# Kernel optimization log

Measured on AMD Instinct MI355X. Metric: run time of the kernel, lower is better.

## Reference

```python
import jax, jax.numpy as jnp
import numpy as np

N_FEAT = 512
N_HEAD = 8
D_K = N_FEAT // N_HEAD


def setup_inputs() -> dict:
    key = jax.random.key(0)
    ks = jax.random.split(key, 10)
    B, S = 2, 4096
    scale = 1.0 / np.sqrt(N_FEAT)
    inp = {
        "x": jax.random.normal(ks[0], (B, S, N_FEAT), dtype=jnp.float32),
        "mask": jnp.zeros((B, 1, 1, S), dtype=jnp.float32),
        "wq": jax.random.normal(ks[1], (N_FEAT, N_FEAT), dtype=jnp.float32) * scale,
        "bq": jnp.zeros((N_FEAT,), dtype=jnp.float32),
        "wk": jax.random.normal(ks[2], (N_FEAT, N_FEAT), dtype=jnp.float32) * scale,
        "bk": jnp.zeros((N_FEAT,), dtype=jnp.float32),
        "wv": jax.random.normal(ks[3], (N_FEAT, N_FEAT), dtype=jnp.float32) * scale,
        "bv": jnp.zeros((N_FEAT,), dtype=jnp.float32),
        "wo": jax.random.normal(ks[4], (N_FEAT, N_FEAT), dtype=jnp.float32) * scale,
        "bo": jnp.zeros((N_FEAT,), dtype=jnp.float32),
    }
    return inp


def reference(x, mask, wq, bq, wk, bk, wv, bv, wo, bo):
    B, S, _ = x.shape
    # QKV projections (weights stored [in, out] = W^T of torch Linear)
    def proj(w, b):
        y = x @ w + b                      # [B, S, n_feat]
        y = y.reshape(B, S, N_HEAD, D_K)
        return y.transpose(0, 2, 1, 3)     # [B, H, S, d_k]
    q = proj(wq, bq)
    k = proj(wk, bk)
    v = proj(wv, bv)
    scores = jnp.einsum("bhsd,bhtd->bhst", q, k) / jnp.sqrt(jnp.float32(D_K))
    scores = scores + mask                 # additive mask, broadcast [B,1,1,S]
    attn = jax.nn.softmax(scores, axis=-1) # [B, H, S, S]
    ctx = jnp.einsum("bhst,bhtd->bhsd", attn, v)
    ctx = ctx.transpose(0, 2, 1, 3).reshape(B, S, N_FEAT)
    return ctx @ wo + bo
```

## Files before the change

kernel.cpp:

```cpp
#include <hip/hip_runtime.h>
#include <hip/hip_bf16.h>
#include <math.h>

#define SLEN 4096
#define NF   512
#define LOG2E 1.44269504f

typedef short s8v  __attribute__((ext_vector_type(8)));
typedef short s4v  __attribute__((ext_vector_type(4)));
typedef float f4v  __attribute__((ext_vector_type(4)));
typedef float f16v __attribute__((ext_vector_type(16)));
typedef __attribute__((address_space(1))) const unsigned int gu32;
typedef __attribute__((address_space(3))) unsigned int lu32;

static __device__ __forceinline__ short f2bf(float f) {
  union { float f; unsigned int u; } v; v.f = f;
  unsigned int u = v.u;
  unsigned int r = (u + 0x7FFFu + ((u >> 16) & 1u)) >> 16;
  return (short)r;
}

__global__ __launch_bounds__(256) void prep_all(
    const float* __restrict__ x, const float* __restrict__ bq,
    const float* __restrict__ mask,
    short* __restrict__ xb, float* __restrict__ bqs, float* __restrict__ maskl) {
  const int b = blockIdx.x, tid = threadIdx.x;
  if (b < 2048) {
    size_t i = ((size_t)b * 256 + tid) * 8;
    float4 a = *(const float4*)(x + i);
    float4 c = *(const float4*)(x + i + 4);
    s8v o;
    o[0] = f2bf(a.x); o[1] = f2bf(a.y); o[2] = f2bf(a.z); o[3] = f2bf(a.w);
    o[4] = f2bf(c.x); o[5] = f2bf(c.y); o[6] = f2bf(c.z); o[7] = f2bf(c.w);
    *(s8v*)(xb + i) = o;
  } else if (b == 2048) {
#pragma unroll
    for (int j = 0; j < 2; j++) {
      int i = tid + 256 * j;
      bqs[i] = bq[i] * (0.125f * LOG2E);
    }
  } else {
    int i4 = ((b - 2049) * 1024) + tid * 4;
    float4 m = *(const float4*)(mask + i4);
    m.x *= LOG2E; m.y *= LOG2E; m.z *= LOG2E; m.w *= LOG2E;
    *(float4*)(maskl + i4) = m;
  }
}

__global__ __launch_bounds__(256) void prep_w(
    const float* __restrict__ wq, const float* __restrict__ wk,
    const float* __restrict__ wv, const float* __restrict__ wo,
    short* __restrict__ wt) {
  const int bz = blockIdx.y;
  const float* W = (bz == 0) ? wq : (bz == 1) ? wk : (bz == 2) ? wv : wo;
  const float scale = (bz == 0) ? 0.125f * LOG2E : 1.0f;
  const int tk = blockIdx.x & 7, tn = blockIdx.x >> 3;
  __shared__ short T[64][68];
  const int tid = threadIdx.x;
#pragma unroll
  for (int p = 0; p < 4; p++) {
    int c = tid + 256 * p;
    int kk = c >> 4, c4 = c & 15;
    float4 v = *(const float4*)(W + (size_t)(tk * 64 + kk) * NF + tn * 64 + c4 * 4);
    T[kk][c4 * 4 + 0] = f2bf(v.x * scale);
    T[kk][c4 * 4 + 1] = f2bf(v.y * scale);
    T[kk][c4 * 4 + 2] = f2bf(v.z * scale);
    T[kk][c4 * 4 + 3] = f2bf(v.w * scale);
  }
  __syncthreads();
#pragma unroll
  for (int p = 0; p < 2; p++) {
    int c = tid + 256 * p;
    int nrow = c >> 3, ks = c & 7;
    s8v g;
#pragma unroll
    for (int j = 0; j < 8; j++) g[j] = T[ks * 8 + j][nrow];
    *(s8v*)(wt + (size_t)bz * NF * NF + (size_t)(tn * 64 + nrow) * NF + tk * 64 + ks * 8) = g;
  }
}

__global__ __launch_bounds__(256) void qkv_proj(
    const short* __restrict__ xb, const short* __restrict__ wt,
    const float* __restrict__ bqs, const float* __restrict__ bk,
    const float* __restrict__ bv,
    short* __restrict__ qo, short* __restrict__ ko, short* __restrict__ vo)
{
  const int z = blockIdx.z;
  const short* WT   = wt + (size_t)z * NF * NF;
  const float* bias = (z == 0) ? bqs : (z == 1) ? bk : bv;
  const int m0 = blockIdx.x * 128;
  const int n0 = blockIdx.y * 128;

  __shared__ short Al[2][128][32];
  __shared__ short Bl[2][128][32];

  const int tid = threadIdx.x;
  const int wave = tid >> 6, lane = tid & 63;
  const int lg = lane >> 4, lr = lane & 15;
  const int wm = wave >> 1, wn = wave & 1;

  const int grow = lane >> 2;
  const int gsl  = lane & 3;

  f4v acc[4][4];
#pragma unroll
  for (int i = 0; i < 4; i++)
#pragma unroll
    for (int j = 0; j < 4; j++) acc[i][j] = (f4v){0.f, 0.f, 0.f, 0.f};

#pragma unroll
  for (int c = 0; c < 2; c++) {
    int row = wave * 32 + c * 16 + grow;
    __builtin_amdgcn_global_load_lds(
        (gu32*)(xb + (size_t)(m0 + row) * NF + gsl * 8),
        (lu32*)&Al[0][wave * 32 + c * 16][0], 16, 0, 0);
    __builtin_amdgcn_global_load_lds(
        (gu32*)(WT + (size_t)(n0 + row) * NF + gsl * 8),
        (lu32*)&Bl[0][wave * 32 + c * 16][0], 16, 0, 0);
  }

#pragma unroll
  for (int ki = 0; ki < 16; ki++) {
    const int cur = ki & 1;
    __syncthreads();

    if (ki + 1 < 16) {
      const int kn = (ki + 1) * 32;
#pragma unroll
      for (int c = 0; c < 2; c++) {
        int row = wave * 32 + c * 16 + grow;
        __builtin_amdgcn_global_load_lds(
            (gu32*)(xb + (size_t)(m0 + row) * NF + kn + gsl * 8),
            (lu32*)&Al[cur ^ 1][wave * 32 + c * 16][0], 16, 0, 0);
        __builtin_amdgcn_global_load_lds(
            (gu32*)(WT + (size_t)(n0 + row) * NF + kn + gsl * 8),
            (lu32*)&Bl[cur ^ 1][wave * 32 + c * 16][0], 16, 0, 0);
      }
    }

    s8v af[4], bf[4];
#pragma unroll
    for (int f = 0; f < 4; f++) af[f] = *(const s8v*)&Al[cur][wm * 64 + f * 16 + lr][lg * 8];
#pragma unroll
    for (int f = 0; f < 4; f++) bf[f] = *(const s8v*)&Bl[cur][wn * 64 + f * 16 + lr][lg * 8];
#pragma unroll
    for (int i = 0; i < 4; i++)
#pragma unroll
      for (int j = 0; j < 4; j++)
        acc[i][j] = __builtin_amdgcn_mfma_f32_16x16x32_bf16(af[i], bf[j], acc[i][j], 0, 0, 0);
  }

#pragma unroll
  for (int i = 0; i < 4; i++) {
    int mbase = m0 + wm * 64 + i * 16 + lg * 4;
#pragma unroll
    for (int j = 0; j < 4; j++) {
      int n = n0 + wn * 64 + j * 16 + lr;
      float bval = bias[n];
      int h = n >> 6, d = n & 63;
      if (z == 2) {
        int b = mbase >> 12, s = mbase & 4095;
        s4v pk;
#pragma unroll
        for (int r = 0; r < 4; r++) pk[r] = f2bf(acc[i][j][r] + bval);
        *(s4v*)(vo + ((size_t)((b * 8 + h) * 64 + d)) * SLEN + s) = pk;
      } else {
        short* dst = (z == 0) ? qo : ko;
#pragma unroll
        for (int r = 0; r < 4; r++) {
          int m = mbase + r;
          int b = m >> 12, s = m & 4095;
          dst[((size_t)((b * 8 + h)) * SLEN + s) * 64 + d] = f2bf(acc[i][j][r] + bval);
        }
      }
    }
  }
}

template<int SPLIT>
__global__ __launch_bounds__(256) void attn(
    const short* __restrict__ q, const short* __restrict__ k,
    const short* __restrict__ vt, const float* __restrict__ maskl,
    short* __restrict__ ctx, float* __restrict__ poa, float* __restrict__ plc)
{
  const int KVLEN = SLEN / SPLIT;
  const int NT = KVLEN / 64;
  __shared__ short Kl[2][64][64];
  __shared__ short Vl[2][64][64];

  const int tid = threadIdx.x;
  const int wave = tid >> 6, lane = tid & 63;
  const int h = lane >> 5, ln = lane & 31;

  const int x = blockIdx.x;
  const int c8 = x & 7, idx = x >> 3;
  const int bhsp = c8 + 8 * (idx >> 5);
  const int qb = idx & 31;
  const int bh = bhsp & 15;
  const int sp = bhsp >> 4;
  const int bb = bh >> 3, hh = bh & 7;
  const int q0 = qb * 128 + wave * 32;

  const short* qp = q + ((size_t)bh * SLEN + q0 + ln) * 64 + h * 8;
  s8v qf[4];
#pragma unroll
  for (int d = 0; d < 4; d++) qf[d] = *(const s8v*)(qp + d * 16);

  s8v ones;
#pragma unroll
  for (int j = 0; j < 8; j++) ones[j] = (short)0x3F80;

  f16v oa[2], lacc;
#pragma unroll
  for (int i = 0; i < 16; i++) { oa[0][i] = 0.f; oa[1][i] = 0.f; lacc[i] = 0.f; }

  const short* kg = k + (size_t)bh * SLEN * 64 + (size_t)sp * KVLEN * 64;
  const short* vg = vt + (size_t)bh * 64 * SLEN + (size_t)sp * KVLEN;
  const float* mp = maskl + (size_t)bb * SLEN + (size_t)sp * KVLEN;

  const int srow = tid >> 3, ss = tid & 7;
  const int sws = (ss ^ (srow & 7)) * 8;

  s8v kr0 = *(const s8v*)(kg + (size_t)srow * 64 + ss * 8);
  s8v kr1 = *(const s8v*)(kg + (size_t)(srow + 32) * 64 + ss * 8);
  s8v vr0 = *(const s8v*)(vg + (size_t)srow * SLEN + ss * 8);
  s8v vr1 = *(const s8v*)(vg + (size_t)(srow + 32) * SLEN + ss * 8);
  *(s8v*)&Kl[0][srow][sws] = kr0;  *(s8v*)&Kl[0][srow + 32][sws] = kr1;
  *(s8v*)&Vl[0][srow][sws] = vr0;  *(s8v*)&Vl[0][srow + 32][sws] = vr1;

  for (int it = 0; it < NT; ++it) {
    const int cur = it & 1;
    const int t0 = it * 64;
    __syncthreads();

    if (it + 1 < NT) {
      kr0 = *(const s8v*)(kg + (size_t)(t0 + 64 + srow) * 64 + ss * 8);
      kr1 = *(const s8v*)(kg + (size_t)(t0 + 96 + srow) * 64 + ss * 8);
      vr0 = *(const s8v*)(vg + (size_t)srow * SLEN + t0 + 64 + ss * 8);
      vr1 = *(const s8v*)(vg + (size_t)(srow + 32) * SLEN + t0 + 64 + ss * 8);
    }

    f16v sa[2];
#pragma unroll
    for (int tt = 0; tt < 2; tt++) {
#pragma unroll
      for (int q4 = 0; q4 < 4; q4++) {
        float4 mv = *(const float4*)(mp + t0 + tt * 32 + q4 * 8 + h * 4);
        sa[tt][q4 * 4 + 0] = mv.x;
        sa[tt][q4 * 4 + 1] = mv.y;
        sa[tt][q4 * 4 + 2] = mv.z;
        sa[tt][q4 * 4 + 3] = mv.w;
      }
    }
    __builtin_amdgcn_s_setprio(1);
#pragma unroll
    for (int tt = 0; tt < 2; tt++) {
#pragma unroll
      for (int ds_ = 0; ds_ < 4; ds_++) {
        s8v kf = *(const s8v*)&Kl[cur][tt * 32 + ln][(((ds_ * 2 + h) ^ (ln & 7))) * 8];
        sa[tt] = __builtin_amdgcn_mfma_f32_32x32x16_bf16(kf, qf[ds_], sa[tt], 0, 0, 0);
      }
    }
    __builtin_amdgcn_s_setprio(0);

    unsigned int pku[2][4][2];
#pragma unroll
    for (int tt = 0; tt < 2; tt++)
#pragma unroll
      for (int q4 = 0; q4 < 4; q4++) {
        float p0, p1, p2, p3;
        asm("v_exp_f32 %0, %1" : "=v"(p0) : "v"(sa[tt][q4 * 4 + 0]));
        asm("v_exp_f32 %0, %1" : "=v"(p1) : "v"(sa[tt][q4 * 4 + 1]));
        asm("v_exp_f32 %0, %1" : "=v"(p2) : "v"(sa[tt][q4 * 4 + 2]));
        asm("v_exp_f32 %0, %1" : "=v"(p3) : "v"(sa[tt][q4 * 4 + 3]));
        unsigned int u0, u1;
        asm("v_cvt_pk_bf16_f32 %0, %1, %2" : "=v"(u0) : "v"(p0), "v"(p1));
        asm("v_cvt_pk_bf16_f32 %0, %1, %2" : "=v"(u1) : "v"(p2), "v"(p3));
        pku[tt][q4][0] = u0;
        pku[tt][q4][1] = u1;
      }

    __builtin_amdgcn_s_setprio(1);
#pragma unroll
    for (int ks = 0; ks < 4; ks++) {
      const int tt = ks >> 1, k1 = ks & 1;
      unsigned int s0 = h ? pku[tt][2 * k1][0] : pku[tt][2 * k1 + 1][0];
      unsigned int s1 = h ? pku[tt][2 * k1][1] : pku[tt][2 * k1 + 1][1];
      unsigned int r0 = (unsigned int)__shfl_xor((int)s0, 32);
      unsigned int r1 = (unsigned int)__shfl_xor((int)s1, 32);
      union { unsigned int u[4]; s8v v; } af;
      af.u[0] = h ? r0 : pku[tt][2 * k1][0];
      af.u[1] = h ? r1 : pku[tt][2 * k1][1];
      af.u[2] = h ? pku[tt][2 * k1 + 1][0] : r0;
      af.u[3] = h ? pku[tt][2 * k1 + 1][1] : r1;
      lacc = __builtin_amdgcn_mfma_f32_32x32x16_bf16(af.v, ones, lacc, 0, 0, 0);
#pragma unroll
      for (int dt = 0; dt < 2; dt++) {
        s8v vf = *(const s8v*)&Vl[cur][dt * 32 + ln][(((ks * 2 + h) ^ (ln & 7))) * 8];
        oa[dt] = __builtin_amdgcn_mfma_f32_32x32x16_bf16(af.v, vf, oa[dt], 0, 0, 0);
      }
    }
    __builtin_amdgcn_s_setprio(0);

    if (it + 1 < NT) {
      *(s8v*)&Kl[cur ^ 1][srow][sws] = kr0;  *(s8v*)&Kl[cur ^ 1][srow + 32][sws] = kr1;
      *(s8v*)&Vl[cur ^ 1][srow][sws] = vr0;  *(s8v*)&Vl[cur ^ 1][srow + 32][sws] = vr1;
    }
  }

  if constexpr (SPLIT == 1) {
#pragma unroll
    for (int q4 = 0; q4 < 4; q4++)
#pragma unroll
      for (int i = 0; i < 4; i++) {
        float inv = 1.0f / lacc[q4 * 4 + i];
        int qrow = q0 + i + q4 * 8 + 4 * h;
        size_t base = ((size_t)bb * SLEN + qrow) * NF + hh * 64;
        ctx[base + ln]      = f2bf(oa[0][q4 * 4 + i] * inv);
        ctx[base + 32 + ln] = f2bf(oa[1][q4 * 4 + i] * inv);
      }
  } else {
#pragma unroll
    for (int dt = 0; dt < 2; dt++) {
      size_t dbase = ((size_t)(sp * 16 + bh) * 64 + dt * 32 + ln) * SLEN;
#pragma unroll
      for (int q4 = 0; q4 < 4; q4++) {
        float4 v = {oa[dt][q4 * 4 + 0], oa[dt][q4 * 4 + 1],
                    oa[dt][q4 * 4 + 2], oa[dt][q4 * 4 + 3]};
        *(float4*)(poa + dbase + q0 + q4 * 8 + 4 * h) = v;
      }
    }
    if (ln == 0) {
      size_t lbase = (size_t)(sp * 16 + bh) * SLEN;
#pragma unroll
      for (int q4 = 0; q4 < 4; q4++) {
        float4 v = {lacc[q4 * 4 + 0], lacc[q4 * 4 + 1],
                    lacc[q4 * 4 + 2], lacc[q4 * 4 + 3]};
        *(float4*)(plc + lbase + q0 + q4 * 8 + 4 * h) = v;
      }
    }
  }
}

__global__ __launch_bounds__(256) void out_proj(
    const short* __restrict__ ctx, const short* __restrict__ wt,
    const float* __restrict__ bo, float* __restrict__ out)
{
  const short* WT = wt + (size_t)3 * NF * NF;
  const int m0 = blockIdx.x * 128;
  const int n0 = blockIdx.y * 128;
  __shared__ short Al[2][128][32];
  __shared__ short Bl[2][128][32];
  const int tid = threadIdx.x;
  const int wave = tid >> 6, lane = tid & 63;
  const int lg = lane >> 4, lr = lane & 15;
  const int wm = wave >> 1, wn = wave & 1;
  const int grow = lane >> 2;
  const int gsl  = lane & 3;

  f4v acc[4][4];
#pragma unroll
  for (int i = 0; i < 4; i++)
#pragma unroll
    for (int j = 0; j < 4; j++) acc[i][j] = (f4v){0.f, 0.f, 0.f, 0.f};

#pragma unroll
  for (int c = 0; c < 2; c++) {
    int row = wave * 32 + c * 16 + grow;
    __builtin_amdgcn_global_load_lds(
        (gu32*)(ctx + (size_t)(m0 + row) * NF + gsl * 8),
        (lu32*)&Al[0][wave * 32 + c * 16][0], 16, 0, 0);
    __builtin_amdgcn_global_load_lds(
        (gu32*)(WT + (size_t)(n0 + row) * NF + gsl * 8),
        (lu32*)&Bl[0][wave * 32 + c * 16][0], 16, 0, 0);
  }

#pragma unroll
  for (int ki = 0; ki < 16; ki++) {
    const int cur = ki & 1;
    __syncthreads();

    if (ki + 1 < 16) {
      const int kn = (ki + 1) * 32;
#pragma unroll
      for (int c = 0; c < 2; c++) {
        int row = wave * 32 + c * 16 + grow;
        __builtin_amdgcn_global_load_lds(
            (gu32*)(ctx + (size_t)(m0 + row) * NF + kn + gsl * 8),
            (lu32*)&Al[cur ^ 1][wave * 32 + c * 16][0], 16, 0, 0);
        __builtin_amdgcn_global_load_lds(
            (gu32*)(WT + (size_t)(n0 + row) * NF + kn + gsl * 8),
            (lu32*)&Bl[cur ^ 1][wave * 32 + c * 16][0], 16, 0, 0);
      }
    }

    s8v af[4], bf[4];
#pragma unroll
    for (int f = 0; f < 4; f++) af[f] = *(const s8v*)&Al[cur][wm * 64 + f * 16 + lr][lg * 8];
#pragma unroll
    for (int f = 0; f < 4; f++) bf[f] = *(const s8v*)&Bl[cur][wn * 64 + f * 16 + lr][lg * 8];
#pragma unroll
    for (int i = 0; i < 4; i++)
#pragma unroll
      for (int j = 0; j < 4; j++)
        acc[i][j] = __builtin_amdgcn_mfma_f32_16x16x32_bf16(af[i], bf[j], acc[i][j], 0, 0, 0);
  }

#pragma unroll
  for (int i = 0; i < 4; i++) {
    int mbase = m0 + wm * 64 + i * 16 + lg * 4;
#pragma unroll
    for (int j = 0; j < 4; j++) {
      int n = n0 + wn * 64 + j * 16 + lr;
      float bval = bo[n];
#pragma unroll
      for (int r = 0; r < 4; r++)
        out[(size_t)(mbase + r) * NF + n] = acc[i][j][r] + bval;
    }
  }
}

extern "C" void kernel_launch(void* const* d_in, const int* in_sizes, int n_in,
                              void* d_out, int out_size, void* d_ws, size_t ws_size,
                              hipStream_t stream) {
  const float* x    = (const float*)d_in[0];
  const float* mask = (const float*)d_in[1];
  const float* wq   = (const float*)d_in[2];
  const float* bq   = (const float*)d_in[3];
  const float* wk   = (const float*)d_in[4];
  const float* bk   = (const float*)d_in[5];
  const float* wv   = (const float*)d_in[6];
  const float* bv   = (const float*)d_in[7];
  const float* wo   = (const float*)d_in[8];
  const float* bo   = (const float*)d_in[9];
  float* out = (float*)d_out;

  char* ws = (char*)d_ws;
  const size_t MB = 1024ull * 1024ull;
  short* xb    = (short*)(ws);
  short* q_ws  = (short*)(ws + 8 * MB);
  short* k_ws  = (short*)(ws + 16 * MB);
  short* v_ws  = (short*)(ws + 24 * MB);
  short* c_ws  = (short*)(ws + 32 * MB);
  short* wt    = (short*)(ws + 40 * MB);
  float* bqs   = (float*)(ws + 42 * MB);
  float* maskl = (float*)(ws + 43 * MB);
  float* poa   = (float*)(ws + 44 * MB);
  float* plc   = (float*)(ws + 76 * MB);

  prep_all<<<2057, 256, 0, stream>>>(x, bq, mask, xb, bqs, maskl);
  prep_w<<<dim3(64, 4), 256, 0, stream>>>(wq, wk, wv, wo, wt);
  qkv_proj<<<dim3(64, 4, 3), 256, 0, stream>>>(xb, wt, bqs, bk, bv, q_ws, k_ws, v_ws);
  attn<1><<<512, 256, 0, stream>>>(q_ws, k_ws, v_ws, maskl, c_ws, poa, plc);
  out_proj<<<dim3(64, 4), 256, 0, stream>>>(c_ws, wt, bo, out);
}
```

Measured before the change: 148.6 us.

## Use 128-key attention tiles and merge weight prep into prep_all launch

The attention kernel now stages 128 keys per iteration instead of 64, so there are half as many loop iterations and block barriers. Each tile is processed as two 64-key halves, with the next tile's prefetch split across those halves. The weight transpose/convert kernel is folded into prep_all as extra blocks, removing one kernel launch. In exchange, shared memory per block doubles (to 64KB), which may lower occupancy, and the XOR swizzle on the 128-wide V rows only covers 8 of the 16 chunks.

```diff
diff --git a/kernel.cpp b/kernel.cpp
--- a/kernel.cpp
+++ b/kernel.cpp
@@ -23,7 +23,11 @@
 __global__ __launch_bounds__(256) void prep_all(
     const float* __restrict__ x, const float* __restrict__ bq,
     const float* __restrict__ mask,
-    short* __restrict__ xb, float* __restrict__ bqs, float* __restrict__ maskl) {
+    const float* __restrict__ wq, const float* __restrict__ wk,
+    const float* __restrict__ wv, const float* __restrict__ wo,
+    short* __restrict__ xb, float* __restrict__ bqs,
+    float* __restrict__ maskl, short* __restrict__ wt) {
+  __shared__ short T[64][68];
   const int b = blockIdx.x, tid = threadIdx.x;
   if (b < 2048) {
     size_t i = ((size_t)b * 256 + tid) * 8;
@@ -39,43 +43,37 @@
       int i = tid + 256 * j;
       bqs[i] = bq[i] * (0.125f * LOG2E);
     }
-  } else {
+  } else if (b < 2057) {
     int i4 = ((b - 2049) * 1024) + tid * 4;
     float4 m = *(const float4*)(mask + i4);
     m.x *= LOG2E; m.y *= LOG2E; m.z *= LOG2E; m.w *= LOG2E;
     *(float4*)(maskl + i4) = m;
-  }
-}
-
-__global__ __launch_bounds__(256) void prep_w(
-    const float* __restrict__ wq, const float* __restrict__ wk,
-    const float* __restrict__ wv, const float* __restrict__ wo,
-    short* __restrict__ wt) {
-  const int bz = blockIdx.y;
-  const float* W = (bz == 0) ? wq : (bz == 1) ? wk : (bz == 2) ? wv : wo;
-  const float scale = (bz == 0) ? 0.125f * LOG2E : 1.0f;
-  const int tk = blockIdx.x & 7, tn = blockIdx.x >> 3;
-  __shared__ short T[64][68];
-  const int tid = threadIdx.x;
-#pragma unroll
-  for (int p = 0; p < 4; p++) {
-    int c = tid + 256 * p;
-    int kk = c >> 4, c4 = c & 15;
-    float4 v = *(const float4*)(W + (size_t)(tk * 64 + kk) * NF + tn * 64 + c4 * 4);
-    T[kk][c4 * 4 + 0] = f2bf(v.x * scale);
-    T[kk][c4 * 4 + 1] = f2bf(v.y * scale);
-    T[kk][c4 * 4 + 2] = f2bf(v.z * scale);
-    T[kk][c4 * 4 + 3] = f2bf(v.w * scale);
-  }
-  __syncthreads();
-#pragma unroll
-  for (int p = 0; p < 2; p++) {
-    int c = tid + 256 * p;
-    int nrow = c >> 3, ks = c & 7;
-    s8v g;
-#pragma unroll
-    for (int j = 0; j < 8; j++) g[j] = T[ks * 8 + j][nrow];
-    *(s8v*)(wt + (size_t)bz * NF * NF + (size_t)(tn * 64 + nrow) * NF + tk * 64 + ks * 8) = g;
+  } else {
+    const int bp = b - 2057;
+    const int bz = bp >> 6, t = bp & 63;
+    const float* W = (bz == 0) ? wq : (bz == 1) ? wk : (bz == 2) ? wv : wo;
+    const float scale = (bz == 0) ? 0.125f * LOG2E : 1.0f;
+    const int tk = t & 7, tn = t >> 3;
+#pragma unroll
+    for (int p = 0; p < 4; p++) {
+      int c = tid + 256 * p;
+      int kk = c >> 4, c4 = c & 15;
+      float4 v = *(const float4*)(W + (size_t)(tk * 64 + kk) * NF + tn * 64 + c4 * 4);
+      T[kk][c4 * 4 + 0] = f2bf(v.x * scale);
+      T[kk][c4 * 4 + 1] = f2bf(v.y * scale);
+      T[kk][c4 * 4 + 2] = f2bf(v.z * scale);
+      T[kk][c4 * 4 + 3] = f2bf(v.w * scale);
+    }
+    __syncthreads();
+#pragma unroll
+    for (int p = 0; p < 2; p++) {
+      int c = tid + 256 * p;
+      int nrow = c >> 3, ks = c & 7;
+      s8v g;
+#pragma unroll
+      for (int j = 0; j < 8; j++) g[j] = T[ks * 8 + j][nrow];
+      *(s8v*)(wt + (size_t)bz * NF * NF + (size_t)(tn * 64 + nrow) * NF + tk * 64 + ks * 8) = g;
+    }
   }
 }
 
@@ -98,7 +96,6 @@
   const int wave = tid >> 6, lane = tid & 63;
   const int lg = lane >> 4, lr = lane & 15;
   const int wm = wave >> 1, wn = wave & 1;
-
   const int grow = lane >> 2;
   const int gsl  = lane & 3;
 
@@ -184,9 +181,9 @@
     short* __restrict__ ctx, float* __restrict__ poa, float* __restrict__ plc)
 {
   const int KVLEN = SLEN / SPLIT;
-  const int NT = KVLEN / 64;
-  __shared__ short Kl[2][64][64];
-  __shared__ short Vl[2][64][64];
+  const int NT = KVLEN / 128;
+  __shared__ short Kl[2][128][64];
+  __shared__ short Vl[2][64][128];
 
   const int tid = threadIdx.x;
   const int wave = tid >> 6, lane = tid & 63;
@@ -218,93 +215,104 @@
   const short* vg = vt + (size_t)bh * 64 * SLEN + (size_t)sp * KVLEN;
   const float* mp = maskl + (size_t)bb * SLEN + (size_t)sp * KVLEN;
 
-  const int srow = tid >> 3, ss = tid & 7;
-  const int sws = (ss ^ (srow & 7)) * 8;
-
-  s8v kr0 = *(const s8v*)(kg + (size_t)srow * 64 + ss * 8);
-  s8v kr1 = *(const s8v*)(kg + (size_t)(srow + 32) * 64 + ss * 8);
-  s8v vr0 = *(const s8v*)(vg + (size_t)srow * SLEN + ss * 8);
-  s8v vr1 = *(const s8v*)(vg + (size_t)(srow + 32) * SLEN + ss * 8);
-  *(s8v*)&Kl[0][srow][sws] = kr0;  *(s8v*)&Kl[0][srow + 32][sws] = kr1;
-  *(s8v*)&Vl[0][srow][sws] = vr0;  *(s8v*)&Vl[0][srow + 32][sws] = vr1;
+  const int tk = tid >> 3, sk = tid & 7;
+  const int dv = tid >> 4, sv = tid & 15;
+  const int swsk = (sk ^ (tk & 7)) * 8;
+  const int swsv = (sv ^ (dv & 7)) * 8;
+
+#pragma unroll
+  for (int p = 0; p < 4; p++) {
+    s8v kr = *(const s8v*)(kg + (size_t)(p * 32 + tk) * 64 + sk * 8);
+    *(s8v*)&Kl[0][p * 32 + tk][swsk] = kr;
+    s8v vr = *(const s8v*)(vg + (size_t)(p * 16 + dv) * SLEN + sv * 8);
+    *(s8v*)&Vl[0][p * 16 + dv][swsv] = vr;
+  }
 
   for (int it = 0; it < NT; ++it) {
     const int cur = it & 1;
-    const int t0 = it * 64;
+    const int t0 = it * 128;
     __syncthreads();
 
-    if (it + 1 < NT) {
-      kr0 = *(const s8v*)(kg + (size_t)(t0 + 64 + srow) * 64 + ss * 8);
-      kr1 = *(const s8v*)(kg + (size_t)(t0 + 96 + srow) * 64 + ss * 8);
-      vr0 = *(const s8v*)(vg + (size_t)srow * SLEN + t0 + 64 + ss * 8);
-      vr1 = *(const s8v*)(vg + (size_t)(srow + 32) * SLEN + t0 + 64 + ss * 8);
-    }
-
-    f16v sa[2];
-#pragma unroll
-    for (int tt = 0; tt < 2; tt++) {
-#pragma unroll
-      for (int q4 = 0; q4 < 4; q4++) {
-        float4 mv = *(const float4*)(mp + t0 + tt * 32 + q4 * 8 + h * 4);
-        sa[tt][q4 * 4 + 0] = mv.x;
-        sa[tt][q4 * 4 + 1] = mv.y;
-        sa[tt][q4 * 4 + 2] = mv.z;
-        sa[tt][q4 * 4 + 3] = mv.w;
-      }
-    }
-    __builtin_amdgcn_s_setprio(1);
-#pragma unroll
-    for (int tt = 0; tt < 2; tt++) {
-#pragma unroll
-      for (int ds_ = 0; ds_ < 4; ds_++) {
-        s8v kf = *(const s8v*)&Kl[cur][tt * 32 + ln][(((ds_ * 2 + h) ^ (ln & 7))) * 8];
-        sa[tt] = __builtin_amdgcn_mfma_f32_32x32x16_bf16(kf, qf[ds_], sa[tt], 0, 0, 0);
-      }
-    }
-    __builtin_amdgcn_s_setprio(0);
-
-    unsigned int pku[2][4][2];
-#pragma unroll
-    for (int tt = 0; tt < 2; tt++)
-#pragma unroll
-      for (int q4 = 0; q4 < 4; q4++) {
-        float p0, p1, p2, p3;
-        asm("v_exp_f32 %0, %1" : "=v"(p0) : "v"(sa[tt][q4 * 4 + 0]));
-        asm("v_exp_f32 %0, %1" : "=v"(p1) : "v"(sa[tt][q4 * 4 + 1]));
-        asm("v_exp_f32 %0, %1" : "=v"(p2) : "v"(sa[tt][q4 * 4 + 2]));
-        asm("v_exp_f32 %0, %1" : "=v"(p3) : "v"(sa[tt][q4 * 4 + 3]));
-        unsigned int u0, u1;
-        asm("v_cvt_pk_bf16_f32 %0, %1, %2" : "=v"(u0) : "v"(p0), "v"(p1));
-        asm("v_cvt_pk_bf16_f32 %0, %1, %2" : "=v"(u1) : "v"(p2), "v"(p3));
-        pku[tt][q4][0] = u0;
-        pku[tt][q4][1] = u1;
-      }
-
-    __builtin_amdgcn_s_setprio(1);
-#pragma unroll
-    for (int ks = 0; ks < 4; ks++) {
-      const int tt = ks >> 1, k1 = ks & 1;
-      unsigned int s0 = h ? pku[tt][2 * k1][0] : pku[tt][2 * k1 + 1][0];
-      unsigned int s1 = h ? pku[tt][2 * k1][1] : pku[tt][2 * k1 + 1][1];
-      unsigned int r0 = (unsigned int)__shfl_xor((int)s0, 32);
-      unsigned int r1 = (unsigned int)__shfl_xor((int)s1, 32);
-      union { unsigned int u[4]; s8v v; } af;
-      af.u[0] = h ? r0 : pku[tt][2 * k1][0];
-      af.u[1] = h ? r1 : pku[tt][2 * k1][1];
-      af.u[2] = h ? pku[tt][2 * k1 + 1][0] : r0;
-      af.u[3] = h ? pku[tt][2 * k1 + 1][1] : r1;
-      lacc = __builtin_amdgcn_mfma_f32_32x32x16_bf16(af.v, ones, lacc, 0, 0, 0);
-#pragma unroll
-      for (int dt = 0; dt < 2; dt++) {
-        s8v vf = *(const s8v*)&Vl[cur][dt * 32 + ln][(((ks * 2 + h) ^ (ln & 7))) * 8];
-        oa[dt] = __builtin_amdgcn_mfma_f32_32x32x16_bf16(af.v, vf, oa[dt], 0, 0, 0);
-      }
-    }
-    __builtin_amdgcn_s_setprio(0);
-
-    if (it + 1 < NT) {
-      *(s8v*)&Kl[cur ^ 1][srow][sws] = kr0;  *(s8v*)&Kl[cur ^ 1][srow + 32][sws] = kr1;
-      *(s8v*)&Vl[cur ^ 1][srow][sws] = vr0;  *(s8v*)&Vl[cur ^ 1][srow + 32][sws] = vr1;
+#pragma unroll
+    for (int hf = 0; hf < 2; hf++) {
+      const int p0 = hf * 2, p1 = hf * 2 + 1;
+      s8v kra, krb, vra, vrb;
+      if (it + 1 < NT) {
+        kra = *(const s8v*)(kg + (size_t)(t0 + 128 + p0 * 32 + tk) * 64 + sk * 8);
+        krb = *(const s8v*)(kg + (size_t)(t0 + 128 + p1 * 32 + tk) * 64 + sk * 8);
+        vra = *(const s8v*)(vg + (size_t)(p0 * 16 + dv) * SLEN + t0 + 128 + sv * 8);
+        vrb = *(const s8v*)(vg + (size_t)(p1 * 16 + dv) * SLEN + t0 + 128 + sv * 8);
+      }
+
+      f16v sa[2];
+#pragma unroll
+      for (int tt = 0; tt < 2; tt++) {
+#pragma unroll
+        for (int q4 = 0; q4 < 4; q4++) {
+          float4 mv = *(const float4*)(mp + t0 + (hf * 2 + tt) * 32 + q4 * 8 + h * 4);
+          sa[tt][q4 * 4 + 0] = mv.x;
+          sa[tt][q4 * 4 + 1] = mv.y;
+          sa[tt][q4 * 4 + 2] = mv.z;
+          sa[tt][q4 * 4 + 3] = mv.w;
+        }
+      }
+      __builtin_amdgcn_s_setprio(1);
+#pragma unroll
+      for (int tt = 0; tt < 2; tt++) {
+#pragma unroll
+        for (int ds_ = 0; ds_ < 4; ds_++) {
+          s8v kf = *(const s8v*)&Kl[cur][(hf * 2 + tt) * 32 + ln][(((ds_ * 2 + h) ^ (ln & 7))) * 8];
+          sa[tt] = __builtin_amdgcn_mfma_f32_32x32x16_bf16(kf, qf[ds_], sa[tt], 0, 0, 0);
+        }
+      }
+      __builtin_amdgcn_s_setprio(0);
+
+      unsigned int pku[2][4][2];
+#pragma unroll
+      for (int tt = 0; tt < 2; tt++)
+#pragma unroll
+        for (int q4 = 0; q4 < 4; q4++) {
+          float p0f, p1f, p2f, p3f;
+          asm("v_exp_f32 %0, %1" : "=v"(p0f) : "v"(sa[tt][q4 * 4 + 0]));
+          asm("v_exp_f32 %0, %1" : "=v"(p1f) : "v"(sa[tt][q4 * 4 + 1]));
+          asm("v_exp_f32 %0, %1" : "=v"(p2f) : "v"(sa[tt][q4 * 4 + 2]));
+          asm("v_exp_f32 %0, %1" : "=v"(p3f) : "v"(sa[tt][q4 * 4 + 3]));
+          unsigned int u0, u1;
+          asm("v_cvt_pk_bf16_f32 %0, %1, %2" : "=v"(u0) : "v"(p0f), "v"(p1f));
+          asm("v_cvt_pk_bf16_f32 %0, %1, %2" : "=v"(u1) : "v"(p2f), "v"(p3f));
+          pku[tt][q4][0] = u0;
+          pku[tt][q4][1] = u1;
+        }
+
+      __builtin_amdgcn_s_setprio(1);
+#pragma unroll
+      for (int kl = 0; kl < 4; kl++) {
+        const int tt = kl >> 1, k1 = kl & 1;
+        const int ks = hf * 4 + kl;
+        unsigned int s0 = h ? pku[tt][2 * k1][0] : pku[tt][2 * k1 + 1][0];
+        unsigned int s1 = h ? pku[tt][2 * k1][1] : pku[tt][2 * k1 + 1][1];
+        unsigned int r0 = (unsigned int)__shfl_xor((int)s0, 32);
+        unsigned int r1 = (unsigned int)__shfl_xor((int)s1, 32);
+        union { unsigned int u[4]; s8v v; } af;
+        af.u[0] = h ? r0 : pku[tt][2 * k1][0];
+        af.u[1] = h ? r1 : pku[tt][2 * k1][1];
+        af.u[2] = h ? pku[tt][2 * k1 + 1][0] : r0;
+        af.u[3] = h ? pku[tt][2 * k1 + 1][1] : r1;
+        lacc = __builtin_amdgcn_mfma_f32_32x32x16_bf16(af.v, ones, lacc, 0, 0, 0);
+#pragma unroll
+        for (int dt = 0; dt < 2; dt++) {
+          s8v vf = *(const s8v*)&Vl[cur][dt * 32 + ln][(((ks * 2 + h) ^ (ln & 7))) * 8];
+          oa[dt] = __builtin_amdgcn_mfma_f32_32x32x16_bf16(af.v, vf, oa[dt], 0, 0, 0);
+        }
+      }
+      __builtin_amdgcn_s_setprio(0);
+
+      if (it + 1 < NT) {
+        *(s8v*)&Kl[cur ^ 1][p0 * 32 + tk][swsk] = kra;
+        *(s8v*)&Kl[cur ^ 1][p1 * 32 + tk][swsk] = krb;
+        *(s8v*)&Vl[cur ^ 1][p0 * 16 + dv][swsv] = vra;
+        *(s8v*)&Vl[cur ^ 1][p1 * 16 + dv][swsv] = vrb;
+      }
     }
   }
 
@@ -448,8 +456,7 @@
   float* poa   = (float*)(ws + 44 * MB);
   float* plc   = (float*)(ws + 76 * MB);
 
-  prep_all<<<2057, 256, 0, stream>>>(x, bq, mask, xb, bqs, maskl);
-  prep_w<<<dim3(64, 4), 256, 0, stream>>>(wq, wk, wv, wo, wt);
+  prep_all<<<2313, 256, 0, stream>>>(x, bq, mask, wq, wk, wv, wo, xb, bqs, maskl, wt);
   qkv_proj<<<dim3(64, 4, 3), 256, 0, stream>>>(xb, wt, bqs, bk, bv, q_ws, k_ws, v_ws);
   attn<1><<<512, 256, 0, stream>>>(q_ws, k_ws, v_ws, maskl, c_ws, poa, plc);
   out_proj<<<dim3(64, 4), 256, 0, stream>>>(c_ws, wt, bo, out);
```

New measurement: 147.0 us. Within noise of the previous version (-1.0%).
